# Optimization experiments

Hardware: AMD Instinct MI355X
Metric: run time of the kernel (lower is better)

Reference implementation:

```python
import jax, jax.numpy as jnp
import numpy as np

B, N, M = 8192, 64, 32          # batch, num_fields, embedding_dim
D = N * (N - 1) // 2            # 2016 pairwise-interaction rows of theta
OUT = 1024                      # block_out_dim
BN_EPS = 1e-5


def setup_inputs() -> dict:
    key = jax.random.key(0)
    k0, k1, k2, k3 = jax.random.split(key, 4)
    inputs = jax.random.normal(k0, (B, N * M), dtype=jnp.float32)
    W_z = jax.random.normal(k1, (N, N, M), dtype=jnp.float32) * 0.05
    theta = jax.random.normal(k2, (D, N), dtype=jnp.float32) * 0.05
    w_affine = jax.random.normal(k3, (OUT, N + D), dtype=jnp.float32) * 0.02
    b_affine = jnp.zeros((OUT,), dtype=jnp.float32)
    gamma = jnp.ones((OUT,), dtype=jnp.float32)
    beta = jnp.zeros((OUT,), dtype=jnp.float32)
    return {"inputs": inputs, "W_z": W_z, "theta": theta,
            "w_affine": w_affine, "b_affine": b_affine,
            "gamma": gamma, "beta": beta}


def reference(inputs, W_z, theta, w_affine, b_affine, gamma, beta):
    b = inputs.shape[0]
    x = inputs.reshape(b, N, M)                      # [B, N, M]
    # lz term: full quadratic form with W_z
    lz = jnp.einsum('bnm,dnm->bd', x, W_z)           # [B, N]
    # lp term: algebraically identical to einsum('bdnm,bdnm->bd') over
    # delta = einsum('bnm,dn->bdnm'): lp[b,d] = sum_n theta[d,n]^2 * sum_m x[b,n,m]^2
    x_sq = jnp.sum(x * x, axis=-1)                   # [B, N]
    lp = x_sq @ (theta * theta).T                    # [B, D]
    out = jnp.concatenate([lz, lp], axis=1)          # [B, N+D]
    out = out @ w_affine.T + b_affine                # [B, OUT]
    # BatchNorm1d in training mode (batch statistics, biased variance)
    mean = jnp.mean(out, axis=0)
    var = jnp.var(out, axis=0)
    out = (out - mean) * jax.lax.rsqrt(var + BN_EPS) * gamma + beta
    return out
```

## Files before the change

### kernel.cpp

```cpp
#include <hip/hip_runtime.h>
#include <stdint.h>

#define NROWS 8192
#define KX    2048
#define KA    2112
#define NF    64
#define DD    2016
#define WCOLS 2080
#define ODIM  1024
#define BN_EPS 1e-5f

#define A1_OT 32
#define A2_DC 8
#define A2_DPC 252
#define A2_OT 16

#define CONV_RPB 4
#define CONV_NB  (NROWS / CONV_RPB)

#define A1A2_A1N 256
#define A1A2_TOT 768

using f32x4  = __attribute__((ext_vector_type(4))) float;
using bf16x8 = __attribute__((ext_vector_type(8))) short;

__device__ __forceinline__ short f2bf(float x) {
    uint32_t u = __float_as_uint(x);
    uint32_t r = (u + 0x7FFFu + ((u >> 16) & 1u)) >> 16;
    return (short)r;
}

__device__ __forceinline__ void gload16(const void* g, void* l) {
    __builtin_amdgcn_global_load_lds(
        (const __attribute__((address_space(1))) uint32_t*)g,
        (__attribute__((address_space(3))) uint32_t*)l, 16, 0, 0);
}

__global__ __launch_bounds__(256) void conv_kern(const float* __restrict__ X,
                                                 short* __restrict__ Xa) {
    const int t = threadIdx.x;
    const int b = blockIdx.x;
#pragma unroll
    for (int r = 0; r < CONV_RPB; ++r) {
        const int row = b * CONV_RPB + r;
        const float4* xr = reinterpret_cast<const float4*>(X + (size_t)row * KX);
        float4 v0 = xr[t * 2];
        float4 v1 = xr[t * 2 + 1];
        bf16x8 s;
        s[0] = f2bf(v0.x); s[1] = f2bf(v0.y); s[2] = f2bf(v0.z); s[3] = f2bf(v0.w);
        s[4] = f2bf(v1.x); s[5] = f2bf(v1.y); s[6] = f2bf(v1.z); s[7] = f2bf(v1.w);
        short* outr = Xa + (size_t)row * KA;
        reinterpret_cast<bf16x8*>(outr)[t] = s;
        float sq = v0.x*v0.x + v0.y*v0.y + v0.z*v0.z + v0.w*v0.w
                 + v1.x*v1.x + v1.y*v1.y + v1.z*v1.z + v1.w*v1.w;
        sq += __shfl_xor(sq, 1);
        sq += __shfl_xor(sq, 2);
        if ((t & 3) == 0) outr[KX + (t >> 2)] = f2bf(sq - 32.0f);
    }
}

__global__ __launch_bounds__(256) void a1a2_kern(short* __restrict__ Aw,
                                                 const float* __restrict__ Wa,
                                                 const float* __restrict__ Wz,
                                                 const float* __restrict__ theta,
                                                 float* __restrict__ partials) {
    const int bid = blockIdx.x;
    const int t = threadIdx.x;
    __shared__ __align__(16) float smem[4096];

    if (bid < A1A2_A1N) {
        const int k = (bid & 7) * 256 + t;
        const int o0 = (bid >> 3) * A1_OT;
        for (int idx = t; idx < A1_OT * 64; idx += 256)
            smem[idx] = Wa[(size_t)(o0 + (idx >> 6)) * WCOLS + (idx & 63)];
        float wz[64];
#pragma unroll
        for (int d = 0; d < 64; ++d) wz[d] = Wz[(size_t)d * KX + k];
        __syncthreads();
#pragma unroll 2
        for (int j = 0; j < A1_OT; ++j) {
            const float* war = &smem[j * 64];
            float acc = 0.f;
#pragma unroll
            for (int d = 0; d < 64; ++d) acc += war[d] * wz[d];
            Aw[(size_t)(o0 + j) * KA + k] = f2bf(acc);
        }
    } else {
        const int b = bid - A1A2_A1N;
        const int n = t & 63;
        const int g = t >> 6;
        const int chunk = b & 7;
        const int o0 = (b >> 3) * A2_OT;
        const int d0 = chunk * A2_DPC;
        float* waT = smem;
        for (int idx = t; idx < A2_OT * A2_DPC; idx += 256) {
            const int j = idx / A2_DPC, dd = idx - j * A2_DPC;
            waT[idx] = Wa[(size_t)(o0 + j) * WCOLS + NF + d0 + dd];
        }
        __syncthreads();
        float acc[A2_OT];
#pragma unroll
        for (int j = 0; j < A2_OT; ++j) acc[j] = 0.f;
        for (int i = g; i < A2_DPC; i += 4) {
            float th = theta[(size_t)(d0 + i) * NF + n];
            float th2 = th * th;
#pragma unroll
            for (int j = 0; j < A2_OT; ++j)
                acc[j] += waT[j * A2_DPC + i] * th2;
        }
        __syncthreads();
        float* red = smem;
#pragma unroll
        for (int j = 0; j < A2_OT; ++j) red[(g * A2_OT + j) * 64 + n] = acc[j];
        __syncthreads();
#pragma unroll
        for (int k2 = 0; k2 < A2_OT * 64 / 256; ++k2) {
            const int idx = t + k2 * 256;
            const int ol = idx >> 6, nn = idx & 63;
            float s = red[(0 * A2_OT + ol) * 64 + nn] + red[(1 * A2_OT + ol) * 64 + nn]
                    + red[(2 * A2_OT + ol) * 64 + nn] + red[(3 * A2_OT + ol) * 64 + nn];
            partials[((size_t)chunk * ODIM + o0 + ol) * NF + nn] = s;
        }
    }
}

__global__ __launch_bounds__(256) void a2_reduce(const float* __restrict__ partials,
                                                 short* __restrict__ Aw) {
    const int idx = blockIdx.x * 256 + threadIdx.x;
    const int o = idx >> 6, n = idx & 63;
    float s = 0.f;
#pragma unroll
    for (int c = 0; c < A2_DC; ++c)
        s += partials[((size_t)c * ODIM + o) * NF + n];
    Aw[(size_t)o * KA + KX + n] = f2bf(s);
}

__global__ __launch_bounds__(256) void gemm_kern(const short* __restrict__ Xa,
                                                 const short* __restrict__ Aw,
                                                 float* __restrict__ C,
                                                 float* __restrict__ sums) {
    __shared__ __align__(16) short As[128 * 32];
    __shared__ __align__(16) short Bs[128 * 32];
    const int tid  = threadIdx.x;
    const int lane = tid & 63;
    const int wid  = tid >> 6;
    const int wr = wid >> 1, wc = wid & 1;
    const int bm = blockIdx.x * 128;
    const int bn = blockIdx.y * 128;

    f32x4 acc[4][4] = {};

    const int c0 = tid, c1 = tid + 256;
    const int r0 = c0 >> 2, q0 = (c0 & 3) ^ ((r0 >> 1) & 3);
    const int r1 = c1 >> 2, q1 = (c1 & 3) ^ ((r1 >> 1) & 3);
    const short* gA0 = Xa + (size_t)(bm + r0) * KA + q0 * 8;
    const short* gA1 = Xa + (size_t)(bm + r1) * KA + q1 * 8;
    const short* gB0 = Aw + (size_t)(bn + r0) * KA + q0 * 8;
    const short* gB1 = Aw + (size_t)(bn + r1) * KA + q1 * 8;
    short* lA0 = As + c0 * 8;  short* lA1 = As + c1 * 8;
    short* lB0 = Bs + c0 * 8;  short* lB1 = Bs + c1 * 8;

    const int lq = lane >> 4;
    int offA[4], offB[4];
#pragma unroll
    for (int m = 0; m < 4; ++m) {
        int ra = wr * 64 + m * 16 + (lane & 15);
        offA[m] = ra * 32 + (lq ^ ((ra >> 1) & 3)) * 8;
        int rb = wc * 64 + m * 16 + (lane & 15);
        offB[m] = rb * 32 + (lq ^ ((rb >> 1) & 3)) * 8;
    }

    for (int kt = 0; kt < KA / 32; ++kt) {
        const int ko = kt * 32;
        gload16(gA0 + ko, lA0);
        gload16(gA1 + ko, lA1);
        gload16(gB0 + ko, lB0);
        gload16(gB1 + ko, lB1);
        __syncthreads();
        bf16x8 a[4], b[4];
#pragma unroll
        for (int m = 0; m < 4; ++m) a[m] = *reinterpret_cast<const bf16x8*>(As + offA[m]);
#pragma unroll
        for (int n = 0; n < 4; ++n) b[n] = *reinterpret_cast<const bf16x8*>(Bs + offB[n]);
#pragma unroll
        for (int m = 0; m < 4; ++m)
#pragma unroll
            for (int n = 0; n < 4; ++n)
                acc[m][n] = __builtin_amdgcn_mfma_f32_16x16x32_bf16(a[m], b[n], acc[m][n], 0, 0, 0);
        __syncthreads();
    }

    const int rlo = (lane >> 4) * 4;
    const int cl  = lane & 15;
#pragma unroll
    for (int n = 0; n < 4; ++n) {
        const int col = bn + wc * 64 + n * 16 + cl;
        float s = 0.f, q = 0.f;
#pragma unroll
        for (int m = 0; m < 4; ++m) {
            const int rowb = bm + wr * 64 + m * 16 + rlo;
#pragma unroll
            for (int r2 = 0; r2 < 4; ++r2) {
                float v = acc[m][n][r2];
                C[(size_t)(rowb + r2) * ODIM + col] = v;
                s += v; q += v * v;
            }
        }
        s += __shfl_xor(s, 16); s += __shfl_xor(s, 32);
        q += __shfl_xor(q, 16); q += __shfl_xor(q, 32);
        if (lane < 16) {
            atomicAdd(&sums[col], s);
            atomicAdd(&sums[ODIM + col], q);
        }
    }
}

__global__ __launch_bounds__(256) void bn_apply(float* __restrict__ C,
                                                const float* __restrict__ sums,
                                                const float* __restrict__ gamma,
                                                const float* __restrict__ beta) {
    const int g = blockIdx.x * 256 + threadIdx.x;
    const int c4 = g & (ODIM / 4 - 1);
    const int row0 = g >> 8;
    const float inv = 1.0f / (float)NROWS;
    float4 sc, sh;
    {
        float4 s0 = reinterpret_cast<const float4*>(sums)[c4];
        float4 q0 = reinterpret_cast<const float4*>(sums + ODIM)[c4];
        float4 gm = reinterpret_cast<const float4*>(gamma)[c4];
        float4 bt = reinterpret_cast<const float4*>(beta)[c4];
        float m, v;
        m = s0.x * inv; v = q0.x * inv - m * m; sc.x = gm.x * rsqrtf(v + BN_EPS); sh.x = bt.x - m * sc.x;
        m = s0.y * inv; v = q0.y * inv - m * m; sc.y = gm.y * rsqrtf(v + BN_EPS); sh.y = bt.y - m * sc.y;
        m = s0.z * inv; v = q0.z * inv - m * m; sc.z = gm.z * rsqrtf(v + BN_EPS); sh.z = bt.z - m * sc.z;
        m = s0.w * inv; v = q0.w * inv - m * m; sc.w = gm.w * rsqrtf(v + BN_EPS); sh.w = bt.w - m * sc.w;
    }
#pragma unroll
    for (int r = 0; r < 4; ++r) {
        const size_t i = (size_t)(row0 + r * 2048) * (ODIM / 4) + c4;
        float4 v = reinterpret_cast<const float4*>(C)[i];
        v.x = v.x * sc.x + sh.x;
        v.y = v.y * sc.y + sh.y;
        v.z = v.z * sc.z + sh.z;
        v.w = v.w * sc.w + sh.w;
        reinterpret_cast<float4*>(C)[i] = v;
    }
}

extern "C" void kernel_launch(void* const* d_in, const int* in_sizes, int n_in,
                              void* d_out, int out_size, void* d_ws, size_t ws_size,
                              hipStream_t stream) {
    const float* X     = (const float*)d_in[0];
    const float* Wz    = (const float*)d_in[1];
    const float* theta = (const float*)d_in[2];
    const float* Wa    = (const float*)d_in[3];
    const float* gamma = (const float*)d_in[5];
    const float* beta  = (const float*)d_in[6];
    float* out = (float*)d_out;

    char* ws = (char*)d_ws;
    float* sums = (float*)ws;
    short* Xa = (short*)(ws + 16384);
    short* Aw = (short*)(ws + 16384 + (size_t)NROWS * KA * 2);
    float* partials = (float*)(ws + 16384 + (size_t)NROWS * KA * 2
                                        + (size_t)ODIM * KA * 2);

    hipMemsetAsync(sums, 0, 2 * ODIM * sizeof(float), stream);
    a1a2_kern<<<A1A2_TOT, 256, 0, stream>>>(Aw, Wa, Wz, theta, partials);
    conv_kern<<<CONV_NB, 256, 0, stream>>>(X, Xa);
    a2_reduce<<<ODIM * NF / 256, 256, 0, stream>>>(partials, Aw);
    gemm_kern<<<dim3(NROWS / 128, ODIM / 128), 256, 0, stream>>>(Xa, Aw, out, sums);
    bn_apply<<<NROWS / 4 * ODIM / 4 / 256, 256, 0, stream>>>(out, sums, gamma, beta);
}
```

Before: 116.4 us.

## Triple-buffer GEMM with 256x128 tiles, BK=64, interleaved prefetch; fuse reduce into conv

The GEMM moves to 256x128 block tiles with 512 threads, a K step of 64 and a triple-buffered LDS pipeline. Global-to-LDS loads for tile kt+2 are interleaved between MFMA groups, with explicit waitcnt, barriers and setprio to overlap memory with compute. The a2_reduce kernel is folded into conv_kern as extra blocks to save a launch. The cost is higher LDS use (about 96KB per block) and a complex hand-tuned barrier schedule that could stall or limit occupancy.

```diff
diff --git a/kernel.cpp b/kernel.cpp
--- a/kernel.cpp
+++ b/kernel.cpp
@@ -17,9 +17,15 @@
 
 #define CONV_RPB 4
 #define CONV_NB  (NROWS / CONV_RPB)
+#define RED_NB   (ODIM * NF / 256)
 
 #define A1A2_A1N 256
 #define A1A2_TOT 768
+
+#define BM 256
+#define BN 128
+#define BK 64
+#define NKT (KA / BK)
 
 using f32x4  = __attribute__((ext_vector_type(4))) float;
 using bf16x8 = __attribute__((ext_vector_type(8))) short;
@@ -36,26 +42,40 @@
         (__attribute__((address_space(3))) uint32_t*)l, 16, 0, 0);
 }
 
+#define MFMA_BF16 __builtin_amdgcn_mfma_f32_16x16x32_bf16
+
 __global__ __launch_bounds__(256) void conv_kern(const float* __restrict__ X,
-                                                 short* __restrict__ Xa) {
+                                                 short* __restrict__ Xa,
+                                                 const float* __restrict__ partials,
+                                                 short* __restrict__ Aw) {
     const int t = threadIdx.x;
     const int b = blockIdx.x;
-#pragma unroll
-    for (int r = 0; r < CONV_RPB; ++r) {
-        const int row = b * CONV_RPB + r;
-        const float4* xr = reinterpret_cast<const float4*>(X + (size_t)row * KX);
-        float4 v0 = xr[t * 2];
-        float4 v1 = xr[t * 2 + 1];
-        bf16x8 s;
-        s[0] = f2bf(v0.x); s[1] = f2bf(v0.y); s[2] = f2bf(v0.z); s[3] = f2bf(v0.w);
-        s[4] = f2bf(v1.x); s[5] = f2bf(v1.y); s[6] = f2bf(v1.z); s[7] = f2bf(v1.w);
-        short* outr = Xa + (size_t)row * KA;
-        reinterpret_cast<bf16x8*>(outr)[t] = s;
-        float sq = v0.x*v0.x + v0.y*v0.y + v0.z*v0.z + v0.w*v0.w
-                 + v1.x*v1.x + v1.y*v1.y + v1.z*v1.z + v1.w*v1.w;
-        sq += __shfl_xor(sq, 1);
-        sq += __shfl_xor(sq, 2);
-        if ((t & 3) == 0) outr[KX + (t >> 2)] = f2bf(sq - 32.0f);
+    if (b < CONV_NB) {
+#pragma unroll
+        for (int r = 0; r < CONV_RPB; ++r) {
+            const int row = b * CONV_RPB + r;
+            const float4* xr = reinterpret_cast<const float4*>(X + (size_t)row * KX);
+            float4 v0 = xr[t * 2];
+            float4 v1 = xr[t * 2 + 1];
+            bf16x8 s;
+            s[0] = f2bf(v0.x); s[1] = f2bf(v0.y); s[2] = f2bf(v0.z); s[3] = f2bf(v0.w);
+            s[4] = f2bf(v1.x); s[5] = f2bf(v1.y); s[6] = f2bf(v1.z); s[7] = f2bf(v1.w);
+            short* outr = Xa + (size_t)row * KA;
+            reinterpret_cast<bf16x8*>(outr)[t] = s;
+            float sq = v0.x*v0.x + v0.y*v0.y + v0.z*v0.z + v0.w*v0.w
+                     + v1.x*v1.x + v1.y*v1.y + v1.z*v1.z + v1.w*v1.w;
+            sq += __shfl_xor(sq, 1);
+            sq += __shfl_xor(sq, 2);
+            if ((t & 3) == 0) outr[KX + (t >> 2)] = f2bf(sq - 32.0f);
+        }
+    } else {
+        const int idx = (b - CONV_NB) * 256 + t;
+        const int o = idx >> 6, n = idx & 63;
+        float s = 0.f;
+#pragma unroll
+        for (int c = 0; c < A2_DC; ++c)
+            s += partials[((size_t)c * ODIM + o) * NF + n];
+        Aw[(size_t)o * KA + KX + n] = f2bf(s);
     }
 }
 
@@ -124,74 +144,165 @@
     }
 }
 
-__global__ __launch_bounds__(256) void a2_reduce(const float* __restrict__ partials,
-                                                 short* __restrict__ Aw) {
-    const int idx = blockIdx.x * 256 + threadIdx.x;
-    const int o = idx >> 6, n = idx & 63;
-    float s = 0.f;
-#pragma unroll
-    for (int c = 0; c < A2_DC; ++c)
-        s += partials[((size_t)c * ODIM + o) * NF + n];
-    Aw[(size_t)o * KA + KX + n] = f2bf(s);
-}
-
-__global__ __launch_bounds__(256) void gemm_kern(const short* __restrict__ Xa,
-                                                 const short* __restrict__ Aw,
-                                                 float* __restrict__ C,
-                                                 float* __restrict__ sums) {
-    __shared__ __align__(16) short As[128 * 32];
-    __shared__ __align__(16) short Bs[128 * 32];
+__global__ __launch_bounds__(512, 2) void gemm_kern(const short* __restrict__ Xa,
+                                                    const short* __restrict__ Aw,
+                                                    float* __restrict__ C,
+                                                    float* __restrict__ sums) {
+    __shared__ __align__(16) short AS[3][BM * BK];
+    __shared__ __align__(16) short BS[3][BN * BK];
     const int tid  = threadIdx.x;
     const int lane = tid & 63;
+    const int cl   = lane & 15;
+    const int kq   = lane >> 4;
     const int wid  = tid >> 6;
-    const int wr = wid >> 1, wc = wid & 1;
-    const int bm = blockIdx.x * 128;
-    const int bn = blockIdx.y * 128;
+    const int wr   = wid >> 1;
+    const int wc   = wid & 1;
+    const int bm = blockIdx.x * BM;
+    const int bn = blockIdx.y * BN;
 
     f32x4 acc[4][4] = {};
 
-    const int c0 = tid, c1 = tid + 256;
-    const int r0 = c0 >> 2, q0 = (c0 & 3) ^ ((r0 >> 1) & 3);
-    const int r1 = c1 >> 2, q1 = (c1 & 3) ^ ((r1 >> 1) & 3);
-    const short* gA0 = Xa + (size_t)(bm + r0) * KA + q0 * 8;
-    const short* gA1 = Xa + (size_t)(bm + r1) * KA + q1 * 8;
-    const short* gB0 = Aw + (size_t)(bn + r0) * KA + q0 * 8;
-    const short* gB1 = Aw + (size_t)(bn + r1) * KA + q1 * 8;
-    short* lA0 = As + c0 * 8;  short* lA1 = As + c1 * 8;
-    short* lB0 = Bs + c0 * 8;  short* lB1 = Bs + c1 * 8;
-
-    const int lq = lane >> 4;
-    int offA[4], offB[4];
+    const short* gAs[4]; int ldA[4];
+    const short* gBs[2]; int ldB[2];
+#pragma unroll
+    for (int i = 0; i < 4; ++i) {
+        const int c = tid + i * 512;
+        const int row = c >> 3, cp = c & 7;
+        gAs[i] = Xa + (size_t)(bm + row) * KA + (cp ^ (row & 7)) * 8;
+        ldA[i] = c * 8;
+    }
+#pragma unroll
+    for (int i = 0; i < 2; ++i) {
+        const int c = tid + i * 512;
+        const int row = c >> 3, cp = c & 7;
+        gBs[i] = Aw + (size_t)(bn + row) * KA + (cp ^ (row & 7)) * 8;
+        ldB[i] = c * 8;
+    }
+
+    int offA[4][2], offB[4][2];
 #pragma unroll
     for (int m = 0; m < 4; ++m) {
-        int ra = wr * 64 + m * 16 + (lane & 15);
-        offA[m] = ra * 32 + (lq ^ ((ra >> 1) & 3)) * 8;
-        int rb = wc * 64 + m * 16 + (lane & 15);
-        offB[m] = rb * 32 + (lq ^ ((rb >> 1) & 3)) * 8;
-    }
-
-    for (int kt = 0; kt < KA / 32; ++kt) {
-        const int ko = kt * 32;
-        gload16(gA0 + ko, lA0);
-        gload16(gA1 + ko, lA1);
-        gload16(gB0 + ko, lB0);
-        gload16(gB1 + ko, lB1);
-        __syncthreads();
-        bf16x8 a[4], b[4];
-#pragma unroll
-        for (int m = 0; m < 4; ++m) a[m] = *reinterpret_cast<const bf16x8*>(As + offA[m]);
-#pragma unroll
-        for (int n = 0; n < 4; ++n) b[n] = *reinterpret_cast<const bf16x8*>(Bs + offB[n]);
-#pragma unroll
-        for (int m = 0; m < 4; ++m)
-#pragma unroll
-            for (int n = 0; n < 4; ++n)
-                acc[m][n] = __builtin_amdgcn_mfma_f32_16x16x32_bf16(a[m], b[n], acc[m][n], 0, 0, 0);
-        __syncthreads();
-    }
-
-    const int rlo = (lane >> 4) * 4;
-    const int cl  = lane & 15;
+        const int r = wr * 64 + m * 16 + cl;
+        offA[m][0] = r * BK + ((kq)     ^ (r & 7)) * 8;
+        offA[m][1] = r * BK + ((4 + kq) ^ (r & 7)) * 8;
+    }
+#pragma unroll
+    for (int n = 0; n < 4; ++n) {
+        const int r = wc * 64 + n * 16 + cl;
+        offB[n][0] = r * BK + ((kq)     ^ (r & 7)) * 8;
+        offB[n][1] = r * BK + ((4 + kq) ^ (r & 7)) * 8;
+    }
+
+#define STAGE_A_PAIR(buf, kt, j) \
+    gload16(gAs[2*(j)]     + (size_t)(kt) * BK, &AS[buf][ldA[2*(j)]]); \
+    gload16(gAs[2*(j) + 1] + (size_t)(kt) * BK, &AS[buf][ldA[2*(j) + 1]]);
+#define STAGE_B_PAIR(buf, kt) \
+    gload16(gBs[0] + (size_t)(kt) * BK, &BS[buf][ldB[0]]); \
+    gload16(gBs[1] + (size_t)(kt) * BK, &BS[buf][ldB[1]]);
+
+    STAGE_A_PAIR(0, 0, 0) STAGE_A_PAIR(0, 0, 1) STAGE_B_PAIR(0, 0)
+    STAGE_A_PAIR(1, 1, 0) STAGE_A_PAIR(1, 1, 1) STAGE_B_PAIR(1, 1)
+    asm volatile("s_waitcnt vmcnt(6)" ::: "memory");
+    __builtin_amdgcn_s_barrier();
+
+    int cb = 0, sb = 2;
+    for (int kt = 0; kt < NKT; ++kt) {
+        const bool st = (kt + 2 < NKT);
+        const short* As = &AS[cb][0];
+        const short* Bs = &BS[cb][0];
+
+        bf16x8 b00 = *(const bf16x8*)(Bs + offB[0][0]);
+        bf16x8 b01 = *(const bf16x8*)(Bs + offB[0][1]);
+        bf16x8 b10 = *(const bf16x8*)(Bs + offB[1][0]);
+        bf16x8 b11 = *(const bf16x8*)(Bs + offB[1][1]);
+        bf16x8 b20 = *(const bf16x8*)(Bs + offB[2][0]);
+        bf16x8 b21 = *(const bf16x8*)(Bs + offB[2][1]);
+        bf16x8 b30 = *(const bf16x8*)(Bs + offB[3][0]);
+        bf16x8 b31 = *(const bf16x8*)(Bs + offB[3][1]);
+        {
+            bf16x8 a0 = *(const bf16x8*)(As + offA[0][0]);
+            bf16x8 a1 = *(const bf16x8*)(As + offA[0][1]);
+            if (st) { STAGE_A_PAIR(sb, kt + 2, 0) }
+            __builtin_amdgcn_s_barrier();
+            asm volatile("s_waitcnt lgkmcnt(0)" ::: "memory");
+            __builtin_amdgcn_sched_barrier(0);
+            __builtin_amdgcn_s_setprio(1);
+            acc[0][0] = MFMA_BF16(a0, b00, acc[0][0], 0, 0, 0);
+            acc[0][0] = MFMA_BF16(a1, b01, acc[0][0], 0, 0, 0);
+            acc[0][1] = MFMA_BF16(a0, b10, acc[0][1], 0, 0, 0);
+            acc[0][1] = MFMA_BF16(a1, b11, acc[0][1], 0, 0, 0);
+            acc[0][2] = MFMA_BF16(a0, b20, acc[0][2], 0, 0, 0);
+            acc[0][2] = MFMA_BF16(a1, b21, acc[0][2], 0, 0, 0);
+            acc[0][3] = MFMA_BF16(a0, b30, acc[0][3], 0, 0, 0);
+            acc[0][3] = MFMA_BF16(a1, b31, acc[0][3], 0, 0, 0);
+            __builtin_amdgcn_s_setprio(0);
+            __builtin_amdgcn_s_barrier();
+        }
+        {
+            bf16x8 a0 = *(const bf16x8*)(As + offA[1][0]);
+            bf16x8 a1 = *(const bf16x8*)(As + offA[1][1]);
+            if (st) { STAGE_A_PAIR(sb, kt + 2, 1) }
+            __builtin_amdgcn_s_barrier();
+            asm volatile("s_waitcnt lgkmcnt(0)" ::: "memory");
+            __builtin_amdgcn_sched_barrier(0);
+            __builtin_amdgcn_s_setprio(1);
+            acc[1][0] = MFMA_BF16(a0, b00, acc[1][0], 0, 0, 0);
+            acc[1][0] = MFMA_BF16(a1, b01, acc[1][0], 0, 0, 0);
+            acc[1][1] = MFMA_BF16(a0, b10, acc[1][1], 0, 0, 0);
+            acc[1][1] = MFMA_BF16(a1, b11, acc[1][1], 0, 0, 0);
+            acc[1][2] = MFMA_BF16(a0, b20, acc[1][2], 0, 0, 0);
+            acc[1][2] = MFMA_BF16(a1, b21, acc[1][2], 0, 0, 0);
+            acc[1][3] = MFMA_BF16(a0, b30, acc[1][3], 0, 0, 0);
+            acc[1][3] = MFMA_BF16(a1, b31, acc[1][3], 0, 0, 0);
+            __builtin_amdgcn_s_setprio(0);
+            __builtin_amdgcn_s_barrier();
+        }
+        {
+            bf16x8 a0 = *(const bf16x8*)(As + offA[2][0]);
+            bf16x8 a1 = *(const bf16x8*)(As + offA[2][1]);
+            if (st) { STAGE_B_PAIR(sb, kt + 2) }
+            __builtin_amdgcn_s_barrier();
+            asm volatile("s_waitcnt lgkmcnt(0)" ::: "memory");
+            __builtin_amdgcn_sched_barrier(0);
+            __builtin_amdgcn_s_setprio(1);
+            acc[2][0] = MFMA_BF16(a0, b00, acc[2][0], 0, 0, 0);
+            acc[2][0] = MFMA_BF16(a1, b01, acc[2][0], 0, 0, 0);
+            acc[2][1] = MFMA_BF16(a0, b10, acc[2][1], 0, 0, 0);
+            acc[2][1] = MFMA_BF16(a1, b11, acc[2][1], 0, 0, 0);
+            acc[2][2] = MFMA_BF16(a0, b20, acc[2][2], 0, 0, 0);
+            acc[2][2] = MFMA_BF16(a1, b21, acc[2][2], 0, 0, 0);
+            acc[2][3] = MFMA_BF16(a0, b30, acc[2][3], 0, 0, 0);
+            acc[2][3] = MFMA_BF16(a1, b31, acc[2][3], 0, 0, 0);
+            __builtin_amdgcn_s_setprio(0);
+            __builtin_amdgcn_s_barrier();
+        }
+        {
+            bf16x8 a0 = *(const bf16x8*)(As + offA[3][0]);
+            bf16x8 a1 = *(const bf16x8*)(As + offA[3][1]);
+            __builtin_amdgcn_s_barrier();
+            asm volatile("s_waitcnt lgkmcnt(0)" ::: "memory");
+            __builtin_amdgcn_sched_barrier(0);
+            __builtin_amdgcn_s_setprio(1);
+            acc[3][0] = MFMA_BF16(a0, b00, acc[3][0], 0, 0, 0);
+            acc[3][0] = MFMA_BF16(a1, b01, acc[3][0], 0, 0, 0);
+            acc[3][1] = MFMA_BF16(a0, b10, acc[3][1], 0, 0, 0);
+            acc[3][1] = MFMA_BF16(a1, b11, acc[3][1], 0, 0, 0);
+            acc[3][2] = MFMA_BF16(a0, b20, acc[3][2], 0, 0, 0);
+            acc[3][2] = MFMA_BF16(a1, b21, acc[3][2], 0, 0, 0);
+            acc[3][3] = MFMA_BF16(a0, b30, acc[3][3], 0, 0, 0);
+            acc[3][3] = MFMA_BF16(a1, b31, acc[3][3], 0, 0, 0);
+            __builtin_amdgcn_s_setprio(0);
+            if (kt < NKT - 1) {
+                if (st) asm volatile("s_waitcnt vmcnt(6)" ::: "memory");
+                else    asm volatile("s_waitcnt vmcnt(0)" ::: "memory");
+            }
+            __builtin_amdgcn_s_barrier();
+        }
+        cb = (cb == 2) ? 0 : cb + 1;
+        sb = (sb == 2) ? 0 : sb + 1;
+    }
+
+    const int rlo = kq * 4;
 #pragma unroll
     for (int n = 0; n < 4; ++n) {
         const int col = bn + wc * 64 + n * 16 + cl;
@@ -267,8 +378,7 @@
 
     hipMemsetAsync(sums, 0, 2 * ODIM * sizeof(float), stream);
     a1a2_kern<<<A1A2_TOT, 256, 0, stream>>>(Aw, Wa, Wz, theta, partials);
-    conv_kern<<<CONV_NB, 256, 0, stream>>>(X, Xa);
-    a2_reduce<<<ODIM * NF / 256, 256, 0, stream>>>(partials, Aw);
-    gemm_kern<<<dim3(NROWS / 128, ODIM / 128), 256, 0, stream>>>(Xa, Aw, out, sums);
+    conv_kern<<<CONV_NB + RED_NB, 256, 0, stream>>>(X, Xa, partials, Aw);
+    gemm_kern<<<dim3(NROWS / BM, ODIM / BN), 512, 0, stream>>>(Xa, Aw, out, sums);
     bn_apply<<<NROWS / 4 * ODIM / 4 / 256, 256, 0, stream>>>(out, sums, gamma, beta);
 }
```

Result: slower. 119.2 us (+2.4%).

## Triple-buffer GEMM LDS loads and fold partial reduce into conversion kernel

Applied to the files above, without the earlier changes.

The GEMM main loop now uses three LDS buffers and issues async global-to-LDS loads two K-tiles ahead. It uses explicit waitcnt and a single barrier per tile instead of load-sync-compute-sync, so memory latency overlaps with MFMA work. Separately, the a2_reduce kernel is merged into conv_kern as extra blocks, which saves one kernel launch. The cost is triple the LDS per block, which may lower occupancy, plus hand-placed wait counts that must match the exact number of outstanding loads.

```diff
diff --git a/kernel.cpp b/kernel.cpp
--- a/kernel.cpp
+++ b/kernel.cpp
@@ -17,9 +17,12 @@
 
 #define CONV_RPB 4
 #define CONV_NB  (NROWS / CONV_RPB)
+#define RED_NB   (ODIM * NF / 256)
 
 #define A1A2_A1N 256
 #define A1A2_TOT 768
+
+#define NT (KA / 32)
 
 using f32x4  = __attribute__((ext_vector_type(4))) float;
 using bf16x8 = __attribute__((ext_vector_type(8))) short;
@@ -36,26 +39,40 @@
         (__attribute__((address_space(3))) uint32_t*)l, 16, 0, 0);
 }
 
+#define MFMA_BF16 __builtin_amdgcn_mfma_f32_16x16x32_bf16
+
 __global__ __launch_bounds__(256) void conv_kern(const float* __restrict__ X,
-                                                 short* __restrict__ Xa) {
+                                                 short* __restrict__ Xa,
+                                                 const float* __restrict__ partials,
+                                                 short* __restrict__ Aw) {
     const int t = threadIdx.x;
     const int b = blockIdx.x;
-#pragma unroll
-    for (int r = 0; r < CONV_RPB; ++r) {
-        const int row = b * CONV_RPB + r;
-        const float4* xr = reinterpret_cast<const float4*>(X + (size_t)row * KX);
-        float4 v0 = xr[t * 2];
-        float4 v1 = xr[t * 2 + 1];
-        bf16x8 s;
-        s[0] = f2bf(v0.x); s[1] = f2bf(v0.y); s[2] = f2bf(v0.z); s[3] = f2bf(v0.w);
-        s[4] = f2bf(v1.x); s[5] = f2bf(v1.y); s[6] = f2bf(v1.z); s[7] = f2bf(v1.w);
-        short* outr = Xa + (size_t)row * KA;
-        reinterpret_cast<bf16x8*>(outr)[t] = s;
-        float sq = v0.x*v0.x + v0.y*v0.y + v0.z*v0.z + v0.w*v0.w
-                 + v1.x*v1.x + v1.y*v1.y + v1.z*v1.z + v1.w*v1.w;
-        sq += __shfl_xor(sq, 1);
-        sq += __shfl_xor(sq, 2);
-        if ((t & 3) == 0) outr[KX + (t >> 2)] = f2bf(sq - 32.0f);
+    if (b < CONV_NB) {
+#pragma unroll
+        for (int r = 0; r < CONV_RPB; ++r) {
+            const int row = b * CONV_RPB + r;
+            const float4* xr = reinterpret_cast<const float4*>(X + (size_t)row * KX);
+            float4 v0 = xr[t * 2];
+            float4 v1 = xr[t * 2 + 1];
+            bf16x8 s;
+            s[0] = f2bf(v0.x); s[1] = f2bf(v0.y); s[2] = f2bf(v0.z); s[3] = f2bf(v0.w);
+            s[4] = f2bf(v1.x); s[5] = f2bf(v1.y); s[6] = f2bf(v1.z); s[7] = f2bf(v1.w);
+            short* outr = Xa + (size_t)row * KA;
+            reinterpret_cast<bf16x8*>(outr)[t] = s;
+            float sq = v0.x*v0.x + v0.y*v0.y + v0.z*v0.z + v0.w*v0.w
+                     + v1.x*v1.x + v1.y*v1.y + v1.z*v1.z + v1.w*v1.w;
+            sq += __shfl_xor(sq, 1);
+            sq += __shfl_xor(sq, 2);
+            if ((t & 3) == 0) outr[KX + (t >> 2)] = f2bf(sq - 32.0f);
+        }
+    } else {
+        const int idx = (b - CONV_NB) * 256 + t;
+        const int o = idx >> 6, n = idx & 63;
+        float s = 0.f;
+#pragma unroll
+        for (int c = 0; c < A2_DC; ++c)
+            s += partials[((size_t)c * ODIM + o) * NF + n];
+        Aw[(size_t)o * KA + KX + n] = f2bf(s);
     }
 }
 
@@ -124,23 +141,12 @@
     }
 }
 
-__global__ __launch_bounds__(256) void a2_reduce(const float* __restrict__ partials,
-                                                 short* __restrict__ Aw) {
-    const int idx = blockIdx.x * 256 + threadIdx.x;
-    const int o = idx >> 6, n = idx & 63;
-    float s = 0.f;
-#pragma unroll
-    for (int c = 0; c < A2_DC; ++c)
-        s += partials[((size_t)c * ODIM + o) * NF + n];
-    Aw[(size_t)o * KA + KX + n] = f2bf(s);
-}
-
 __global__ __launch_bounds__(256) void gemm_kern(const short* __restrict__ Xa,
                                                  const short* __restrict__ Aw,
                                                  float* __restrict__ C,
                                                  float* __restrict__ sums) {
-    __shared__ __align__(16) short As[128 * 32];
-    __shared__ __align__(16) short Bs[128 * 32];
+    __shared__ __align__(16) short As[3][128 * 32];
+    __shared__ __align__(16) short Bs[3][128 * 32];
     const int tid  = threadIdx.x;
     const int lane = tid & 63;
     const int wid  = tid >> 6;
@@ -157,8 +163,7 @@
     const short* gA1 = Xa + (size_t)(bm + r1) * KA + q1 * 8;
     const short* gB0 = Aw + (size_t)(bn + r0) * KA + q0 * 8;
     const short* gB1 = Aw + (size_t)(bn + r1) * KA + q1 * 8;
-    short* lA0 = As + c0 * 8;  short* lA1 = As + c1 * 8;
-    short* lB0 = Bs + c0 * 8;  short* lB1 = Bs + c1 * 8;
+    const int l0 = c0 * 8, l1 = c1 * 8;
 
     const int lq = lane >> 4;
     int offA[4], offB[4];
@@ -170,25 +175,49 @@
         offB[m] = rb * 32 + (lq ^ ((rb >> 1) & 3)) * 8;
     }
 
-    for (int kt = 0; kt < KA / 32; ++kt) {
-        const int ko = kt * 32;
-        gload16(gA0 + ko, lA0);
-        gload16(gA1 + ko, lA1);
-        gload16(gB0 + ko, lB0);
-        gload16(gB1 + ko, lB1);
-        __syncthreads();
-        bf16x8 a[4], b[4];
-#pragma unroll
-        for (int m = 0; m < 4; ++m) a[m] = *reinterpret_cast<const bf16x8*>(As + offA[m]);
-#pragma unroll
-        for (int n = 0; n < 4; ++n) b[n] = *reinterpret_cast<const bf16x8*>(Bs + offB[n]);
-#pragma unroll
-        for (int m = 0; m < 4; ++m)
-#pragma unroll
-            for (int n = 0; n < 4; ++n)
-                acc[m][n] = __builtin_amdgcn_mfma_f32_16x16x32_bf16(a[m], b[n], acc[m][n], 0, 0, 0);
-        __syncthreads();
-    }
+#define STAGE(buf, kt) do {                         \
+        const int ko_ = (kt) * 32;                  \
+        gload16(gA0 + ko_, &As[buf][l0]);           \
+        gload16(gA1 + ko_, &As[buf][l1]);           \
+        gload16(gB0 + ko_, &Bs[buf][l0]);           \
+        gload16(gB1 + ko_, &Bs[buf][l1]);           \
+    } while (0)
+
+#define TILE(cbuf, sbuf, kt) do {                                          \
+        if ((kt) + 2 < NT) STAGE(sbuf, (kt) + 2);                          \
+        bf16x8 a_[4], b_[4];                                               \
+        _Pragma("unroll")                                                  \
+        for (int m = 0; m < 4; ++m)                                        \
+            a_[m] = *reinterpret_cast<const bf16x8*>(&As[cbuf][offA[m]]);  \
+        _Pragma("unroll")                                                  \
+        for (int n = 0; n < 4; ++n)                                        \
+            b_[n] = *reinterpret_cast<const bf16x8*>(&Bs[cbuf][offB[n]]);  \
+        asm volatile("s_waitcnt lgkmcnt(0)" ::: "memory");                 \
+        __builtin_amdgcn_sched_barrier(0);                                 \
+        _Pragma("unroll")                                                  \
+        for (int m = 0; m < 4; ++m)                                        \
+            _Pragma("unroll")                                              \
+            for (int n = 0; n < 4; ++n)                                    \
+                acc[m][n] = MFMA_BF16(a_[m], b_[n], acc[m][n], 0, 0, 0);   \
+        if ((kt) + 2 < NT)                                                 \
+            asm volatile("s_waitcnt vmcnt(4)" ::: "memory");               \
+        else if ((kt) + 1 < NT)                                            \
+            asm volatile("s_waitcnt vmcnt(0)" ::: "memory");               \
+        __builtin_amdgcn_s_barrier();                                      \
+    } while (0)
+
+    STAGE(0, 0);
+    STAGE(1, 1);
+    asm volatile("s_waitcnt vmcnt(4)" ::: "memory");
+    __builtin_amdgcn_s_barrier();
+
+    for (int kt = 0; kt < NT; kt += 3) {
+        TILE(0, 2, kt);
+        TILE(1, 0, kt + 1);
+        TILE(2, 1, kt + 2);
+    }
+#undef TILE
+#undef STAGE
 
     const int rlo = (lane >> 4) * 4;
     const int cl  = lane & 15;
@@ -267,8 +296,7 @@
 
     hipMemsetAsync(sums, 0, 2 * ODIM * sizeof(float), stream);
     a1a2_kern<<<A1A2_TOT, 256, 0, stream>>>(Aw, Wa, Wz, theta, partials);
-    conv_kern<<<CONV_NB, 256, 0, stream>>>(X, Xa);
-    a2_reduce<<<ODIM * NF / 256, 256, 0, stream>>>(partials, Aw);
+    conv_kern<<<CONV_NB + RED_NB, 256, 0, stream>>>(X, Xa, partials, Aw);
     gemm_kern<<<dim3(NROWS / 128, ODIM / 128), 256, 0, stream>>>(Xa, Aw, out, sums);
     bn_apply<<<NROWS / 4 * ODIM / 4 / 256, 256, 0, stream>>>(out, sums, gamma, beta);
 }
```

After: 114.8 us. Within noise of the previous version (-1.4%).
